# Performance work log

Measured on AMD Instinct MI355X. Metric: run time of the kernel, lower is better.

## Reference

```python
import jax, jax.numpy as jnp
import numpy as np

B, S, D, H = 4, 2048, 1024, 16
DK = D // H
NEG = -1e9  # stand-in for -inf; keeps softmax grads NaN-free, same math after softmax


def setup_inputs() -> dict:
    key = jax.random.key(0)
    ks = jax.random.split(key, 8)
    scale = 0.02
    return {
        "q": jax.random.normal(ks[0], (B, S, D), jnp.float32),
        "k": jax.random.normal(ks[1], (B, S, D), jnp.float32),
        "v": jax.random.normal(ks[2], (B, S, D), jnp.float32),
        "mask": jnp.ones((B, S), jnp.int32),
        "Wq": jax.random.normal(ks[3], (D, D), jnp.float32) * scale,
        "bq": jnp.zeros((D,), jnp.float32),
        "Wk": jax.random.normal(ks[4], (D, D), jnp.float32) * scale,
        "bk": jnp.zeros((D,), jnp.float32),
        "Wv": jax.random.normal(ks[5], (D, D), jnp.float32) * scale,
        "bv": jnp.zeros((D,), jnp.float32),
        "Wp": jax.random.normal(ks[6], (D, D), jnp.float32) * scale,
        "bp": jnp.zeros((D,), jnp.float32),
    }


def reference(q, k, v, mask, Wq, bq, Wk, bk, Wv, bv, Wp, bp):
    # torch.nn.Linear: y = x @ W.T + b
    Q = q @ Wq.T + bq  # [B,S,D]
    K = k @ Wk.T + bk
    V = v @ Wv.T + bv
    # split heads -> [B,H,S,dk]
    Q = Q.reshape(B, S, H, DK).transpose(0, 2, 1, 3)
    K = K.reshape(B, S, H, DK).transpose(0, 2, 1, 3)
    V = V.reshape(B, S, H, DK).transpose(0, 2, 1, 3)
    Sc = jnp.einsum("bhqd,bhkd->bhqk", Q, K) / jnp.sqrt(jnp.float32(DK))
    # padding mask: [B,1,1,Sk]
    Sc = jnp.where(mask[:, None, None, :] == 0, NEG, Sc)
    # causal mask (tril), as in the registered buffer
    causal = jnp.tril(jnp.ones((S, S), jnp.bool_))
    Sc = jnp.where(causal, Sc, NEG)
    A = jax.nn.softmax(Sc, axis=-1)  # attn_drop with p=0 is identity
    x = jnp.einsum("bhqk,bhkd->bhqd", A, V)
    x = x.transpose(0, 2, 1, 3).reshape(B, S, D)
    return x @ Wp.T + bp
```

## Files before the change

kernel.cpp:

```cpp
#include <hip/hip_runtime.h>
#include <stdint.h>


#define SZB (8192u * 1024u * 2u)
#define WSZ (1024u * 1024u * 2u)
#define NKT 16
#define SLOT 24576

typedef __attribute__((ext_vector_type(8))) short  short8;
typedef __attribute__((ext_vector_type(4))) short  short4v;
typedef __attribute__((ext_vector_type(4))) float  f32x4;

#define MFMA16(a, b, c) __builtin_amdgcn_mfma_f32_16x16x32_bf16(a, b, c, 0, 0, 0)

__device__ __forceinline__ f32x4 mfma_k16(short4v a, short4v b, f32x4 c) {
#if __has_builtin(__builtin_amdgcn_mfma_f32_16x16x16bf16_1k)
  return __builtin_amdgcn_mfma_f32_16x16x16bf16_1k(a, b, c, 0, 0, 0);
#else
  asm volatile("v_mfma_f32_16x16x16_bf16 %0, %1, %2, %0"
               : "+v"(c) : "v"(a), "v"(b));
  return c;
#endif
}
__device__ __forceinline__ uint32_t cvtpk(float a, float b) {
  uint32_t r;
  asm("v_cvt_pk_bf16_f32 %0, %1, %2" : "=v"(r) : "v"(a), "v"(b));
  return r;
}

__device__ __forceinline__ ushort f2bf(float f) {
  uint32_t u = __float_as_uint(f);
  u += 0x7FFF + ((u >> 16) & 1);
  return (ushort)(u >> 16);
}
__device__ __forceinline__ short8 cvt8(float4 a, float4 b) {
  short8 r;
  r[0] = (short)f2bf(a.x); r[1] = (short)f2bf(a.y);
  r[2] = (short)f2bf(a.z); r[3] = (short)f2bf(a.w);
  r[4] = (short)f2bf(b.x); r[5] = (short)f2bf(b.y);
  r[6] = (short)f2bf(b.z); r[7] = (short)f2bf(b.w);
  return r;
}
__device__ __forceinline__ void gl_lds16(const ushort* g, ushort* l) {
  __builtin_amdgcn_global_load_lds(
      (__attribute__((address_space(1))) void*)g,
      (__attribute__((address_space(3))) void*)l, 16, 0, 0);
}

__global__ __launch_bounds__(256) void cvt_w(
    const float* __restrict__ Wq, const float* __restrict__ Wk,
    const float* __restrict__ Wv, const float* __restrict__ Wp,
    ushort* __restrict__ Wqb, ushort* __restrict__ Wkb,
    ushort* __restrict__ Wvb, ushort* __restrict__ Wpb) {
  const int z = blockIdx.y;
  const float* s = (z == 0) ? Wq : (z == 1) ? Wk : (z == 2) ? Wv : Wp;
  ushort* d = (z == 0) ? Wqb : (z == 1) ? Wkb : (z == 2) ? Wvb : Wpb;
  const size_t i = (size_t)(blockIdx.x * 256 + threadIdx.x) * 8;
  *(short8*)&d[i] = cvt8(*(const float4*)&s[i], *(const float4*)&s[i + 4]);
}

__global__ __launch_bounds__(256) void cvt_in(
    const float* __restrict__ q, const float* __restrict__ k,
    const float* __restrict__ v,
    ushort* __restrict__ qb2, ushort* __restrict__ kb2,
    ushort* __restrict__ vb2) {
  const int z = blockIdx.y;
  const float* s = (z == 0) ? q : (z == 1) ? k : v;
  ushort* d = (z == 0) ? qb2 : (z == 1) ? kb2 : vb2;
  const size_t i = (size_t)(blockIdx.x * 256 + threadIdx.x) * 8;
  *(short8*)&d[i] = cvt8(*(const float4*)&s[i], *(const float4*)&s[i + 4]);
}

__device__ __forceinline__ void core8p(
    const ushort* __restrict__ A, const ushort* __restrict__ Wb,
    ushort* lds, int m0, int n0, f32x4 acc[4][4]) {
  const int tid  = threadIdx.x;
  const int w    = tid >> 6;
  const int lane = tid & 63;
  const int quad = lane >> 4;
  const int l16  = lane & 15;
  const int wm   = (w >> 1) * 64;
  const int wn   = (w & 1) * 64;

  const ushort* asrc[4];
  const ushort* bsrc[2];
#pragma unroll
  for (int i = 0; i < 4; ++i) {
    const int c = tid + 512 * i;
    asrc[i] = A + (size_t)(m0 + (c >> 3)) * 1024 + ((c & 7) ^ ((c >> 3) & 7)) * 8;
  }
#pragma unroll
  for (int i = 0; i < 2; ++i) {
    const int c = tid + 512 * i;
    bsrc[i] = Wb + (size_t)(n0 + (c >> 3)) * 1024 + ((c & 7) ^ ((c >> 3) & 7)) * 8;
  }

  auto stage = [&](int j, int s) {
    ushort* base = lds + s * SLOT + w * 512;
#pragma unroll
    for (int i = 0; i < 4; ++i)
      gl_lds16(asrc[i] + j * 64, base + i * 4096);
#pragma unroll
    for (int i = 0; i < 2; ++i)
      gl_lds16(bsrc[i] + j * 64, base + 16384 + i * 4096);
  };

  const int rsw = (l16 & 7) * 8;
  auto compute = [&](int s) {
    const ushort* pA = lds + s * SLOT;
    const ushort* pB = pA + 16384;
    short8 a[4][2], b[4][2];
#pragma unroll
    for (int f = 0; f < 4; ++f)
#pragma unroll
      for (int ks = 0; ks < 2; ++ks) {
        a[f][ks] = *(const short8*)&pA[(wm + f * 16 + l16) * 64 +
                                       ((ks * 32 + quad * 8) ^ rsw)];
        b[f][ks] = *(const short8*)&pB[(wn + f * 16 + l16) * 64 +
                                       ((ks * 32 + quad * 8) ^ rsw)];
      }
    __builtin_amdgcn_s_setprio(1);
#pragma unroll
    for (int i = 0; i < 4; ++i)
#pragma unroll
      for (int j2 = 0; j2 < 4; ++j2) {
        acc[i][j2] = MFMA16(a[i][0], b[j2][0], acc[i][j2]);
        acc[i][j2] = MFMA16(a[i][1], b[j2][1], acc[i][j2]);
      }
    __builtin_amdgcn_s_setprio(0);
  };

  stage(0, 0);
  stage(1, 1);
  int s = 0;
#pragma unroll 1
  for (int j = 0; j < NKT - 1; ++j) {
    asm volatile("s_waitcnt vmcnt(6)" ::: "memory");
    __builtin_amdgcn_s_barrier();
    __builtin_amdgcn_sched_barrier(0);
    if (j < NKT - 2) {
      int s2 = s + 2; if (s2 >= 3) s2 -= 3;
      stage(j + 2, s2);
    }
    compute(s);
    if (++s == 3) s = 0;
  }
  asm volatile("s_waitcnt vmcnt(0)" ::: "memory");
  __builtin_amdgcn_s_barrier();
  __builtin_amdgcn_sched_barrier(0);
  compute(s);
}

__global__ __launch_bounds__(512, 2) void gemm_qkv8(
    const ushort* __restrict__ qb2, const ushort* __restrict__ kb2,
    const ushort* __restrict__ vb2,
    const ushort* __restrict__ Wqb, const ushort* __restrict__ Wkb,
    const ushort* __restrict__ Wvb,
    const float* __restrict__ bq, const float* __restrict__ bk,
    const float* __restrict__ bv,
    ushort* __restrict__ Qb, ushort* __restrict__ Kb, ushort* __restrict__ Vt) {
  __shared__ ushort lds[3 * SLOT];

  const int z = blockIdx.z;
  const ushort* A    = (z == 0) ? qb2 : (z == 1) ? kb2 : vb2;
  const ushort* W    = (z == 0) ? Wqb : (z == 1) ? Wkb : Wvb;
  const float*  bias = (z == 0) ? bq  : (z == 1) ? bk  : bv;

  const int m0 = blockIdx.x * 256;
  const int n0 = blockIdx.y * 128;

  f32x4 acc[4][4] = {};
  core8p(A, W, lds, m0, n0, acc);

  const int tid  = threadIdx.x;
  const int w    = tid >> 6;
  const int lane = tid & 63;
  const int quad = lane >> 4;
  const int l16  = lane & 15;
  const int wm   = (w >> 1) * 64;
  const int wn   = (w & 1) * 64;

  float bvv[4];
#pragma unroll
  for (int j = 0; j < 4; ++j) bvv[j] = bias[n0 + wn + j * 16 + l16];

  if (z < 2) {
    ushort* Out = (z == 0) ? Qb : Kb;
    const float sc = (z == 0) ? 0.1803368801f : 1.0f;
#pragma unroll
    for (int i = 0; i < 4; ++i) {
      const int m = m0 + wm + i * 16 + quad * 4;
#pragma unroll
      for (int j = 0; j < 4; ++j) {
        const int n = n0 + wn + j * 16 + l16;
#pragma unroll
        for (int r = 0; r < 4; ++r)
          Out[(size_t)(m + r) * 1024 + n] = f2bf((acc[i][j][r] + bvv[j]) * sc);
      }
    }
  } else {
#pragma unroll
    for (int i = 0; i < 4; ++i) {
      const int mrow = m0 + wm + i * 16 + quad * 4;
      const int bb   = mrow >> 11;
      const int s0   = mrow & 2047;
#pragma unroll
      for (int j = 0; j < 4; ++j) {
        const int n = n0 + wn + j * 16 + l16;
        ushort4 pk;
        pk.x = f2bf(acc[i][j][0] + bvv[j]);
        pk.y = f2bf(acc[i][j][1] + bvv[j]);
        pk.z = f2bf(acc[i][j][2] + bvv[j]);
        pk.w = f2bf(acc[i][j][3] + bvv[j]);
        *(ushort4*)&Vt[(size_t)((bb * 16 + (n >> 6)) * 64 + (n & 63)) * 2048 + s0] = pk;
      }
    }
  }
}

__global__ __launch_bounds__(512, 2) void gemm_proj8(
    const ushort* __restrict__ Xin, const ushort* __restrict__ Wpb,
    const float* __restrict__ bp, float* __restrict__ Out) {
  __shared__ ushort lds[3 * SLOT];

  const int m0 = blockIdx.x * 256;
  const int n0 = blockIdx.y * 128;

  f32x4 acc[4][4] = {};
  core8p(Xin, Wpb, lds, m0, n0, acc);

  const int tid  = threadIdx.x;
  const int w    = tid >> 6;
  const int lane = tid & 63;
  const int quad = lane >> 4;
  const int l16  = lane & 15;
  const int wm   = (w >> 1) * 64;
  const int wn   = (w & 1) * 64;

  float bvv[4];
#pragma unroll
  for (int j = 0; j < 4; ++j) bvv[j] = bp[n0 + wn + j * 16 + l16];

#pragma unroll
  for (int i = 0; i < 4; ++i) {
    const int m = m0 + wm + i * 16 + quad * 4;
#pragma unroll
    for (int j = 0; j < 4; ++j) {
      const int n = n0 + wn + j * 16 + l16;
#pragma unroll
      for (int r = 0; r < 4; ++r)
        Out[(size_t)(m + r) * 1024 + n] = acc[i][j][r] + bvv[j];
    }
  }
}

__global__ __launch_bounds__(256) void gemm_v_fb(
    const float* __restrict__ vin, const ushort* __restrict__ Wvb,
    const float* __restrict__ bv, ushort* __restrict__ Vt) {
  __shared__ ushort As[128 * 32];
  __shared__ ushort Bs[128 * 32];

  const int tid  = threadIdx.x;
  const int w    = tid >> 6;
  const int lane = tid & 63;
  const int quad = lane >> 4;
  const int l16  = lane & 15;
  const int wm   = (w >> 1) * 64;
  const int wn   = (w & 1) * 64;
  const int r0   = tid >> 2;
  const int r1   = r0 + 64;
  const int c0   = (tid & 3) * 8;

  const int m0 = blockIdx.x * 128;
  const int n0 = blockIdx.y * 128;

  f32x4 acc[4][4] = {};
  const ushort* Wg = Wvb + (size_t)(n0 + w * 32 + (lane >> 2)) * 1024 + (lane & 3) * 8;
  const float*  Ag0 = vin + (size_t)(m0 + r0) * 1024 + c0;
  const float*  Ag1 = vin + (size_t)(m0 + r1) * 1024 + c0;

  float4 p0a = *(const float4*)(Ag0), p0b = *(const float4*)(Ag0 + 4);
  float4 p1a = *(const float4*)(Ag1), p1b = *(const float4*)(Ag1 + 4);

  for (int kt = 0; kt < 32; ++kt) {
    const int ko = kt * 32;
    __syncthreads();
    *(short8*)&As[r0 * 32 + c0] = cvt8(p0a, p0b);
    *(short8*)&As[r1 * 32 + c0] = cvt8(p1a, p1b);
    gl_lds16(Wg + ko,         &Bs[(w * 32) * 32]);
    gl_lds16(Wg + 16384 + ko, &Bs[(w * 32 + 16) * 32]);
    __syncthreads();
    if (kt < 31) {
      const int kn = ko + 32;
      p0a = *(const float4*)(Ag0 + kn); p0b = *(const float4*)(Ag0 + kn + 4);
      p1a = *(const float4*)(Ag1 + kn); p1b = *(const float4*)(Ag1 + kn + 4);
    }
    short8 af[4], bfr[4];
#pragma unroll
    for (int i = 0; i < 4; ++i)
      af[i] = *(const short8*)&As[(wm + i * 16 + l16) * 32 + quad * 8];
#pragma unroll
    for (int i = 0; i < 4; ++i)
      bfr[i] = *(const short8*)&Bs[(wn + i * 16 + l16) * 32 + quad * 8];
#pragma unroll
    for (int i = 0; i < 4; ++i)
#pragma unroll
      for (int j = 0; j < 4; ++j)
        acc[i][j] = MFMA16(af[i], bfr[j], acc[i][j]);
  }

  float bvv[4];
#pragma unroll
  for (int j = 0; j < 4; ++j) bvv[j] = bv[n0 + wn + j * 16 + l16];
#pragma unroll
  for (int i = 0; i < 4; ++i) {
    const int mrow = m0 + wm + i * 16 + quad * 4;
    const int bb   = mrow >> 11;
    const int s0   = mrow & 2047;
#pragma unroll
    for (int j = 0; j < 4; ++j) {
      const int n = n0 + wn + j * 16 + l16;
      ushort4 pk;
      pk.x = f2bf(acc[i][j][0] + bvv[j]);
      pk.y = f2bf(acc[i][j][1] + bvv[j]);
      pk.z = f2bf(acc[i][j][2] + bvv[j]);
      pk.w = f2bf(acc[i][j][3] + bvv[j]);
      *(ushort4*)&Vt[(size_t)((bb * 16 + (n >> 6)) * 64 + (n & 63)) * 2048 + s0] = pk;
    }
  }
}

__global__ __launch_bounds__(256, 4) void attn(
    ushort* __restrict__ Qb, const ushort* __restrict__ Kb,
    const ushort* __restrict__ Vt, const int* __restrict__ mask) {
  __shared__ ushort Ks[64 * 68];
  __shared__ ushort Vts[64 * 68];

  const int wgid = (int)blockIdx.x + 16 * (int)blockIdx.y;
  const int xcd  = wgid & 7;
  const int idx  = wgid >> 3;
  const int bh   = xcd * 8 + (idx >> 4);
  const int pair = idx & 15;
  const int b = bh >> 4, h = bh & 15;
  const int tid = threadIdx.x, w = tid >> 6, lane = tid & 63;
  const int quad = lane >> 4, l16 = lane & 15;
  const int ql = w * 16 + l16;

  short8 kst[2], vst[2];
  int mld;

  auto ld_tile = [&](int k0) {
#pragma unroll
    for (int i = 0; i < 2; ++i) {
      const int c = tid + 256 * i;
      kst[i] = *(const short8*)&Kb[(size_t)(b * 2048 + k0 + (c >> 3)) * 1024 +
                                   h * 64 + (c & 7) * 8];
      vst[i] = *(const short8*)&Vt[(size_t)(bh * 64 + (c >> 3)) * 2048 +
                                   k0 + (c & 7) * 8];
    }
    mld = mask[b * 2048 + k0 + lane];
  };

#pragma unroll 1
  for (int seg = 0; seg < 2; ++seg) {
    const int qt = seg ? (31 - pair) : pair;
    const int q0 = qt * 64;

    const size_t qoff = (size_t)(b * 2048 + q0 + w * 16 + l16) * 1024 + h * 64 + quad * 8;
    const short8 qf0 = *(const short8*)&Qb[qoff];
    const short8 qf1 = *(const short8*)&Qb[qoff + 32];

    f32x4 oacc[4] = {};
    float lsum[4] = {0.f, 0.f, 0.f, 0.f};

    ld_tile(0);

    for (int kt = 0; kt <= qt; ++kt) {
      __syncthreads();
#pragma unroll
      for (int i = 0; i < 2; ++i) {
        const int c = tid + 256 * i;
        *(short8*)&Ks[(c >> 3) * 68 + (c & 7) * 8]  = kst[i];
        *(short8*)&Vts[(c >> 3) * 68 + (c & 7) * 8] = vst[i];
      }
      const int mcur = mld;
      __syncthreads();

      if (kt < qt) ld_tile((kt + 1) * 64);

      const unsigned long long mbits = __ballot(mcur != 0);
      const bool allm = (mbits == ~0ull);

      f32x4 sc[4];
#pragma unroll
      for (int nj = 0; nj < 4; ++nj) {
        f32x4 z4 = {0.f, 0.f, 0.f, 0.f};
        const short8 kf0 = *(const short8*)&Ks[(nj * 16 + l16) * 68 + quad * 8];
        const short8 kf1 = *(const short8*)&Ks[(nj * 16 + l16) * 68 + 32 + quad * 8];
        z4 = MFMA16(kf0, qf0, z4);
        z4 = MFMA16(kf1, qf1, z4);
        sc[nj] = z4;
      }

      float pv[4][4];
      if (kt < qt) {
        if (allm) {
#pragma unroll
          for (int nj = 0; nj < 4; ++nj)
#pragma unroll
            for (int r = 0; r < 4; ++r)
              pv[nj][r] = __builtin_amdgcn_exp2f(sc[nj][r]);
        } else {
#pragma unroll
          for (int nj = 0; nj < 4; ++nj) {
            const uint32_t sub = (uint32_t)(mbits >> (nj * 16));
#pragma unroll
            for (int r = 0; r < 4; ++r) {
              const bool ok = (sub >> (quad * 4 + r)) & 1;
              pv[nj][r] = __builtin_amdgcn_exp2f(ok ? sc[nj][r] : -1e5f);
            }
          }
        }
      } else {
#pragma unroll
        for (int nj = 0; nj < 4; ++nj) {
          const uint32_t sub = allm ? 0xffffffffu : (uint32_t)(mbits >> (nj * 16));
#pragma unroll
          for (int r = 0; r < 4; ++r) {
            const int kl = nj * 16 + quad * 4 + r;
            const bool ok = ((sub >> (quad * 4 + r)) & 1) && (kl <= ql);
            pv[nj][r] = __builtin_amdgcn_exp2f(ok ? sc[nj][r] : -1e5f);
          }
        }
      }
#pragma unroll
      for (int nj = 0; nj < 4; ++nj)
#pragma unroll
        for (int r = 0; r < 4; ++r) lsum[r] += pv[nj][r];

      short4v pa[4];
#pragma unroll
      for (int nj = 0; nj < 4; ++nj) {
        uint32_t u0 = cvtpk(pv[nj][0], pv[nj][1]);
        uint32_t u1 = cvtpk(pv[nj][2], pv[nj][3]);
        pa[nj][0] = (short)(u0 & 0xffff); pa[nj][1] = (short)(u0 >> 16);
        pa[nj][2] = (short)(u1 & 0xffff); pa[nj][3] = (short)(u1 >> 16);
      }

#pragma unroll
      for (int nj = 0; nj < 4; ++nj)
#pragma unroll
        for (int nb = 0; nb < 4; ++nb) {
          const short4v vf = *(const short4v*)&Vts[(nb * 16 + l16) * 68 +
                                                   nj * 16 + quad * 4];
          oacc[nb] = mfma_k16(pa[nj], vf, oacc[nb]);
        }
    }

    float v = lsum[0] + lsum[1] + lsum[2] + lsum[3];
    v += __shfl_xor(v, 16);
    v += __shfl_xor(v, 32);
    const float inv = 1.0f / v;
    float invr[4];
#pragma unroll
    for (int r = 0; r < 4; ++r) invr[r] = __shfl(inv, quad * 4 + r);

#pragma unroll
    for (int nb = 0; nb < 4; ++nb)
#pragma unroll
      for (int r = 0; r < 4; ++r) {
        const int q = q0 + w * 16 + quad * 4 + r;
        Qb[(size_t)(b * 2048 + q) * 1024 + h * 64 + nb * 16 + l16] =
            f2bf(oacc[nb][r] * invr[r]);
      }
  }
}

extern "C" void kernel_launch(void* const* d_in, const int* in_sizes, int n_in,
                              void* d_out, int out_size, void* d_ws, size_t ws_size,
                              hipStream_t stream) {
  const float* q    = (const float*)d_in[0];
  const float* k    = (const float*)d_in[1];
  const float* v    = (const float*)d_in[2];
  const int*   mask = (const int*)d_in[3];
  const float* Wq   = (const float*)d_in[4];
  const float* bq   = (const float*)d_in[5];
  const float* Wk   = (const float*)d_in[6];
  const float* bk   = (const float*)d_in[7];
  const float* Wv   = (const float*)d_in[8];
  const float* bv   = (const float*)d_in[9];
  const float* Wp   = (const float*)d_in[10];
  const float* bp   = (const float*)d_in[11];
  float* out = (float*)d_out;

  char* ws = (char*)d_ws;
  ushort* Qb  = (ushort*)(ws);
  ushort* Kb  = (ushort*)(ws + (size_t)SZB);
  ushort* Vt  = (ushort*)(ws + (size_t)2 * SZB);
  ushort* Wqb = (ushort*)(ws + (size_t)3 * SZB);
  ushort* Wkb = (ushort*)(ws + (size_t)3 * SZB + WSZ);
  ushort* Wvb = (ushort*)(ws + (size_t)3 * SZB + 2 * WSZ);
  ushort* Wpb = (ushort*)(ws + (size_t)3 * SZB + 3 * WSZ);

  ushort* qb2 = (ushort*)out;
  ushort* kb2 = (ushort*)((char*)out + (size_t)SZB);
  const size_t need_v = (size_t)3 * SZB + 4 * WSZ + SZB;
  const int v_bf = (ws_size >= need_v) ? 1 : 0;
  ushort* vb2 = v_bf ? (ushort*)(ws + (size_t)3 * SZB + 4 * WSZ) : nullptr;

  cvt_w<<<dim3(512, 4), dim3(256), 0, stream>>>(Wq, Wk, Wv, Wp, Wqb, Wkb, Wvb, Wpb);
  cvt_in<<<dim3(4096, 2 + v_bf), dim3(256), 0, stream>>>(q, k, v, qb2, kb2, vb2);
  gemm_qkv8<<<dim3(32, 8, 2 + v_bf), dim3(512), 0, stream>>>(
      qb2, kb2, vb2, Wqb, Wkb, Wvb, bq, bk, bv, Qb, Kb, Vt);
  if (!v_bf)
    gemm_v_fb<<<dim3(64, 8), dim3(256), 0, stream>>>(v, Wvb, bv, Vt);
  attn<<<dim3(16, 64), dim3(256), 0, stream>>>(Qb, Kb, Vt, mask);
  gemm_proj8<<<dim3(32, 8), dim3(512), 0, stream>>>(Qb, Wpb, bp, out);
}
```

Baseline: 311.2 us.

## Split attention waves 2x2 over query rows and key columns with LDS reduction

```diff
diff --git a/kernel.cpp b/kernel.cpp
--- a/kernel.cpp
+++ b/kernel.cpp
@@ -335,6 +335,8 @@
     const ushort* __restrict__ Vt, const int* __restrict__ mask) {
   __shared__ ushort Ks[64 * 68];
   __shared__ ushort Vts[64 * 68];
+  __shared__ f32x4  red[16 * 64];
+  __shared__ float  sml[2][2][2][16];
 
   const int wgid = (int)blockIdx.x + 16 * (int)blockIdx.y;
   const int xcd  = wgid & 7;
@@ -344,7 +346,7 @@
   const int b = bh >> 4, h = bh & 15;
   const int tid = threadIdx.x, w = tid >> 6, lane = tid & 63;
   const int quad = lane >> 4, l16 = lane & 15;
-  const int ql = w * 16 + l16;
+  const int wq = w >> 1, wk = w & 1;
 
   short8 kst[2], vst[2];
   int mld;
@@ -366,12 +368,17 @@
     const int qt = seg ? (31 - pair) : pair;
     const int q0 = qt * 64;
 
-    const size_t qoff = (size_t)(b * 2048 + q0 + w * 16 + l16) * 1024 + h * 64 + quad * 8;
-    const short8 qf0 = *(const short8*)&Qb[qoff];
-    const short8 qf1 = *(const short8*)&Qb[qoff + 32];
-
-    f32x4 oacc[4] = {};
-    float lsum[4] = {0.f, 0.f, 0.f, 0.f};
+    short8 qf[2][2];
+#pragma unroll
+    for (int qc = 0; qc < 2; ++qc) {
+      const size_t qoff = (size_t)(b * 2048 + q0 + wq * 32 + qc * 16 + l16) * 1024 +
+                          h * 64 + quad * 8;
+      qf[qc][0] = *(const short8*)&Qb[qoff];
+      qf[qc][1] = *(const short8*)&Qb[qoff + 32];
+    }
+
+    f32x4 oacc[2][4] = {};
+    float lsum[2] = {0.f, 0.f};
 
     ld_tile(0);
 
@@ -391,88 +398,122 @@
       const unsigned long long mbits = __ballot(mcur != 0);
       const bool allm = (mbits == ~0ull);
 
-      f32x4 sc[4];
-#pragma unroll
-      for (int nj = 0; nj < 4; ++nj) {
-        f32x4 z4 = {0.f, 0.f, 0.f, 0.f};
-        const short8 kf0 = *(const short8*)&Ks[(nj * 16 + l16) * 68 + quad * 8];
-        const short8 kf1 = *(const short8*)&Ks[(nj * 16 + l16) * 68 + 32 + quad * 8];
-        z4 = MFMA16(kf0, qf0, z4);
-        z4 = MFMA16(kf1, qf1, z4);
-        sc[nj] = z4;
-      }
-
-      float pv[4][4];
-      if (kt < qt) {
-        if (allm) {
-#pragma unroll
-          for (int nj = 0; nj < 4; ++nj)
+      f32x4 sc[2][2];
+#pragma unroll
+      for (int kg = 0; kg < 2; ++kg) {
+        const short8 kf0 = *(const short8*)&Ks[(wk * 32 + kg * 16 + l16) * 68 + quad * 8];
+        const short8 kf1 = *(const short8*)&Ks[(wk * 32 + kg * 16 + l16) * 68 + 32 + quad * 8];
+#pragma unroll
+        for (int qc = 0; qc < 2; ++qc) {
+          f32x4 z4 = {0.f, 0.f, 0.f, 0.f};
+          z4 = MFMA16(kf0, qf[qc][0], z4);
+          z4 = MFMA16(kf1, qf[qc][1], z4);
+          sc[kg][qc] = z4;
+        }
+      }
+
+      float pv[2][2][4];
+      if (kt < qt && allm) {
+#pragma unroll
+        for (int kg = 0; kg < 2; ++kg)
+#pragma unroll
+          for (int qc = 0; qc < 2; ++qc)
 #pragma unroll
             for (int r = 0; r < 4; ++r)
-              pv[nj][r] = __builtin_amdgcn_exp2f(sc[nj][r]);
-        } else {
-#pragma unroll
-          for (int nj = 0; nj < 4; ++nj) {
-            const uint32_t sub = (uint32_t)(mbits >> (nj * 16));
+              pv[kg][qc][r] = __builtin_amdgcn_exp2f(sc[kg][qc][r]);
+      } else if (kt < qt) {
+#pragma unroll
+        for (int kg = 0; kg < 2; ++kg) {
+          const uint32_t sub = (uint32_t)(mbits >> (wk * 32 + kg * 16));
+#pragma unroll
+          for (int qc = 0; qc < 2; ++qc)
 #pragma unroll
             for (int r = 0; r < 4; ++r) {
               const bool ok = (sub >> (quad * 4 + r)) & 1;
-              pv[nj][r] = __builtin_amdgcn_exp2f(ok ? sc[nj][r] : -1e5f);
+              pv[kg][qc][r] = __builtin_amdgcn_exp2f(ok ? sc[kg][qc][r] : -1e5f);
             }
+        }
+      } else {
+#pragma unroll
+        for (int kg = 0; kg < 2; ++kg) {
+          const uint32_t sub = allm ? 0xffffffffu
+                                    : (uint32_t)(mbits >> (wk * 32 + kg * 16));
+#pragma unroll
+          for (int qc = 0; qc < 2; ++qc)
+#pragma unroll
+            for (int r = 0; r < 4; ++r) {
+              const int kl   = wk * 32 + kg * 16 + quad * 4 + r;
+              const int qlcl = wq * 32 + qc * 16 + l16;
+              const bool ok = (((sub >> (quad * 4 + r)) & 1) != 0) && (kl <= qlcl);
+              pv[kg][qc][r] = __builtin_amdgcn_exp2f(ok ? sc[kg][qc][r] : -1e5f);
+            }
+        }
+      }
+#pragma unroll
+      for (int kg = 0; kg < 2; ++kg)
+#pragma unroll
+        for (int qc = 0; qc < 2; ++qc)
+#pragma unroll
+          for (int r = 0; r < 4; ++r) lsum[qc] += pv[kg][qc][r];
+
+      short4v pa[2][2];
+#pragma unroll
+      for (int kg = 0; kg < 2; ++kg)
+#pragma unroll
+        for (int qc = 0; qc < 2; ++qc) {
+          const uint32_t u0 = cvtpk(pv[kg][qc][0], pv[kg][qc][1]);
+          const uint32_t u1 = cvtpk(pv[kg][qc][2], pv[kg][qc][3]);
+          pa[kg][qc][0] = (short)(u0 & 0xffff); pa[kg][qc][1] = (short)(u0 >> 16);
+          pa[kg][qc][2] = (short)(u1 & 0xffff); pa[kg][qc][3] = (short)(u1 >> 16);
+        }
+
+#pragma unroll
+      for (int kg = 0; kg < 2; ++kg)
+#pragma unroll
+        for (int nb = 0; nb < 4; ++nb) {
+          const short4v vf = *(const short4v*)&Vts[(nb * 16 + l16) * 68 +
+                                                   wk * 32 + kg * 16 + quad * 4];
+#pragma unroll
+          for (int qc = 0; qc < 2; ++qc)
+            oacc[qc][nb] = mfma_k16(pa[kg][qc], vf, oacc[qc][nb]);
+        }
+    }
+
+#pragma unroll
+    for (int qc = 0; qc < 2; ++qc) {
+      float vv = lsum[qc];
+      vv += __shfl_xor(vv, 16);
+      vv += __shfl_xor(vv, 32);
+      if (quad == 0) sml[wq][wk][qc][l16] = vv;
+    }
+    if (wk == 1) {
+#pragma unroll
+      for (int qc = 0; qc < 2; ++qc)
+#pragma unroll
+        for (int nb = 0; nb < 4; ++nb)
+          red[((wq * 2 + qc) * 4 + nb) * 64 + lane] = oacc[qc][nb];
+    }
+    __syncthreads();
+    if (wk == 0) {
+#pragma unroll
+      for (int qc = 0; qc < 2; ++qc) {
+        const float tot = sml[wq][0][qc][l16] + sml[wq][1][qc][l16];
+        const float inv = 1.0f / tot;
+        float invr[4];
+#pragma unroll
+        for (int r = 0; r < 4; ++r) invr[r] = __shfl(inv, quad * 4 + r);
+#pragma unroll
+        for (int nb = 0; nb < 4; ++nb) {
+          const f32x4 o2 = red[((wq * 2 + qc) * 4 + nb) * 64 + lane];
+#pragma unroll
+          for (int r = 0; r < 4; ++r) {
+            const int qrow = q0 + wq * 32 + qc * 16 + quad * 4 + r;
+            Qb[(size_t)(b * 2048 + qrow) * 1024 + h * 64 + nb * 16 + l16] =
+                f2bf((oacc[qc][nb][r] + o2[r]) * invr[r]);
           }
         }
-      } else {
-#pragma unroll
-        for (int nj = 0; nj < 4; ++nj) {
-          const uint32_t sub = allm ? 0xffffffffu : (uint32_t)(mbits >> (nj * 16));
-#pragma unroll
-          for (int r = 0; r < 4; ++r) {
-            const int kl = nj * 16 + quad * 4 + r;
-            const bool ok = ((sub >> (quad * 4 + r)) & 1) && (kl <= ql);
-            pv[nj][r] = __builtin_amdgcn_exp2f(ok ? sc[nj][r] : -1e5f);
-          }
-        }
-      }
-#pragma unroll
-      for (int nj = 0; nj < 4; ++nj)
-#pragma unroll
-        for (int r = 0; r < 4; ++r) lsum[r] += pv[nj][r];
-
-      short4v pa[4];
-#pragma unroll
-      for (int nj = 0; nj < 4; ++nj) {
-        uint32_t u0 = cvtpk(pv[nj][0], pv[nj][1]);
-        uint32_t u1 = cvtpk(pv[nj][2], pv[nj][3]);
-        pa[nj][0] = (short)(u0 & 0xffff); pa[nj][1] = (short)(u0 >> 16);
-        pa[nj][2] = (short)(u1 & 0xffff); pa[nj][3] = (short)(u1 >> 16);
-      }
-
-#pragma unroll
-      for (int nj = 0; nj < 4; ++nj)
-#pragma unroll
-        for (int nb = 0; nb < 4; ++nb) {
-          const short4v vf = *(const short4v*)&Vts[(nb * 16 + l16) * 68 +
-                                                   nj * 16 + quad * 4];
-          oacc[nb] = mfma_k16(pa[nj], vf, oacc[nb]);
-        }
-    }
-
-    float v = lsum[0] + lsum[1] + lsum[2] + lsum[3];
-    v += __shfl_xor(v, 16);
-    v += __shfl_xor(v, 32);
-    const float inv = 1.0f / v;
-    float invr[4];
-#pragma unroll
-    for (int r = 0; r < 4; ++r) invr[r] = __shfl(inv, quad * 4 + r);
-
-#pragma unroll
-    for (int nb = 0; nb < 4; ++nb)
-#pragma unroll
-      for (int r = 0; r < 4; ++r) {
-        const int q = q0 + w * 16 + quad * 4 + r;
-        Qb[(size_t)(b * 2048 + q) * 1024 + h * 64 + nb * 16 + l16] =
-            f2bf(oacc[nb][r] * invr[r]);
-      }
+      }
+    }
   }
 }
 
```

New measurement: 311.4 us. About the same (+0.0%).
